# Kernel tuning notes

Hardware: AMD Instinct MI355X
Metric: run time of the kernel (lower is better)

## Reference

```python
import jax, jax.numpy as jnp
import numpy as np

B = 64        # batch
L = 256       # latent_dim
H = 1024      # hidden
D = 1024      # mask dim
BAND = 16     # half-bandwidth of sparsity mask
M = 2 * BAND + 1  # max nnz per row (=33)


def _banded_mask_idx():
    """Build a banded (D,D) 0/1 mask and per-row column indices (D,M), -1 padded."""
    r = np.arange(D)
    mask = (np.abs(r[:, None] - r[None, :]) <= BAND).astype(np.float32)
    idx = np.full((D, M), -1, dtype=np.int32)
    for i in range(D):
        cols = np.nonzero(mask[i])[0]
        idx[i, :len(cols)] = cols
    return mask, idx


def setup_inputs() -> dict:
    key = jax.random.key(0)
    kz, k1, kb1, k2, kb2 = jax.random.split(key, 5)
    mask_np, idx_np = _banded_mask_idx()
    return {
        "z": jax.random.normal(kz, (B, L), dtype=jnp.float32),
        "mask": jnp.asarray(mask_np),
        "W1": jax.random.normal(k1, (L, H), dtype=jnp.float32) * 0.05,
        "b1": jax.random.normal(kb1, (H,), dtype=jnp.float32) * 0.05,
        "W2": jax.random.normal(k2, (H, D * M), dtype=jnp.float32) * 0.02,
        "b2": jax.random.normal(kb2, (D * M,), dtype=jnp.float32) * 0.02,
        "idx": jnp.asarray(idx_np),
    }


def reference(z, mask, W1, b1, W2, b2, idx):
    b = z.shape[0]
    # 2-layer MLP with exact (erf) GELU, as in nn.GELU()
    h = jax.nn.gelu(z @ W1 + b1, approximate=False)
    v = (h @ W2 + b2).reshape(b, D, M)          # (B, D, M)
    # scatter predicted values onto the mask support (unique targets -> add == set)
    valid = idx >= 0                             # (D, M)
    jc = jnp.where(valid, idx, 0)                # clamp -1 padding to col 0
    rows = jnp.broadcast_to(jnp.arange(D)[:, None], (D, M))
    vals = jnp.where(valid, v, jnp.zeros((), v.dtype))
    k = jnp.zeros((b, D, D), dtype=z.dtype).at[:, rows, jc].add(vals)
    # symmetrize, add identity, re-apply mask
    k = 0.5 * (k + jnp.swapaxes(k, -1, -2))
    k = k + jnp.eye(D, dtype=z.dtype)
    return k * mask[None, :, :]
```

## Files before the change

### kernel.cpp

```cpp
#include <hip/hip_runtime.h>
#include <math.h>

#define BATCH 64
#define LDIM  256
#define HDIM  1024
#define DDIM  1024
#define BAND  16
#define MNZ   33
#define NN    (DDIM*MNZ)
#define RTILE 64
#define LSTR  34

typedef float v4f __attribute__((ext_vector_type(4)));

__global__ __launch_bounds__(256) void k1_h(const float* __restrict__ z,
                                            const float* __restrict__ W1,
                                            const float* __restrict__ b1,
                                            float* __restrict__ ht) {
    __shared__ float zs[LDIM];
    const int t = threadIdx.x;
    const int b = blockIdx.y;
    const int j = blockIdx.x * 256 + t;
    zs[t] = z[b * LDIM + t];
    __syncthreads();
    float acc = b1[j];
#pragma unroll 8
    for (int l = 0; l < LDIM; ++l)
        acc = fmaf(zs[l], W1[l * HDIM + j], acc);
    float g = 0.5f * acc * (1.0f + erff(acc * 0.70710678118654752f));
    ht[(size_t)j * BATCH + b] = g;
}

__global__ __launch_bounds__(256) void k2_v(const float* __restrict__ W2,
                                            const float* __restrict__ b2,
                                            const float* __restrict__ ht,
                                            float* __restrict__ vpart,
                                            int kchunk) {
    const int lane = threadIdx.x & 63;
    const int wave = __builtin_amdgcn_readfirstlane((int)(threadIdx.x >> 6));
    const int c0 = blockIdx.x * 256 + lane * 4;
    const int b0 = wave * 16;
    const int ks = blockIdx.y * kchunk;

    v4f acc[16];
#pragma unroll
    for (int j = 0; j < 16; ++j) acc[j] = (v4f){0.f, 0.f, 0.f, 0.f};

    const float* __restrict__ wp = W2 + (size_t)ks * NN + c0;
    const float* __restrict__ hp = ht + (size_t)ks * BATCH + b0;

#pragma unroll 2
    for (int kk = 0; kk < kchunk; ++kk) {
        const v4f w4 = *(const v4f*)(wp + (size_t)kk * NN);
        const float* __restrict__ hh = hp + (size_t)kk * BATCH;
#pragma unroll
        for (int j = 0; j < 16; ++j)
            acc[j] += hh[j] * w4;
    }

    float* __restrict__ vo = vpart + (size_t)blockIdx.y * (BATCH * (size_t)NN)
                             + (size_t)b0 * NN + c0;
    if (blockIdx.y == 0) {
        const v4f bias = *(const v4f*)(b2 + c0);
#pragma unroll
        for (int j = 0; j < 16; ++j)
            *(v4f*)(vo + (size_t)j * NN) = acc[j] + bias;
    } else {
#pragma unroll
        for (int j = 0; j < 16; ++j)
            *(v4f*)(vo + (size_t)j * NN) = acc[j];
    }
}

__global__ __launch_bounds__(256) void k3_out(const float* __restrict__ vpart,
                                              float* __restrict__ out,
                                              int nsplit) {
    const int tid  = threadIdx.x;
    const int tile = blockIdx.x & (DDIM / RTILE - 1);
    const int b    = blockIdx.x / (DDIM / RTILE);
    const int i0 = tile * RTILE;
    const int js = (i0 >= BAND) ? (i0 - BAND) : 0;
    const int je = (i0 + RTILE + BAND <= DDIM) ? (i0 + RTILE + BAND) : DDIM;
    const int nelem = (je - js) * MNZ;

    __shared__ float ls[(RTILE + 2 * BAND) * LSTR];

    const float* __restrict__ vb = vpart + (size_t)b * NN + (size_t)js * MNZ;
    const size_t slice = (size_t)BATCH * NN;
    for (int idx = tid; idx < nelem; idx += 256) {
        const int r = idx / MNZ;
        const int m = idx - r * MNZ;
        float s = vb[idx];
        for (int sl = 1; sl < nsplit; ++sl)
            s += vb[(size_t)sl * slice + idx];
        ls[r * LSTR + m] = s;
    }
    __syncthreads();

    const int j0 = tid * 4;
    for (int r = 0; r < RTILE; ++r) {
        const int i = i0 + r;
        v4f res = (v4f){0.f, 0.f, 0.f, 0.f};
        if (j0 + 3 >= i - BAND && j0 <= i + BAND) {
            const int lo_i = (i > BAND) ? (i - BAND) : 0;
#pragma unroll
            for (int c = 0; c < 4; ++c) {
                const int j = j0 + c;
                const int d = j - i;
                float x = 0.0f;
                if (d >= -BAND && d <= BAND) {
                    const int lo_j = (j > BAND) ? (j - BAND) : 0;
                    x = 0.5f * (ls[(i - js) * LSTR + (j - lo_i)] +
                                ls[(j - js) * LSTR + (i - lo_j)]);
                    if (d == 0) x += 1.0f;
                }
                res[c] = x;
            }
        }
        v4f* dst = ((v4f*)out) + ((size_t)b * DDIM + i) * (DDIM / 4) + tid;
        __builtin_nontemporal_store(res, dst);
    }
}

extern "C" void kernel_launch(void* const* d_in, const int* in_sizes, int n_in,
                              void* d_out, int out_size, void* d_ws, size_t ws_size,
                              hipStream_t stream) {
    const float* z  = (const float*)d_in[0];
    const float* W1 = (const float*)d_in[2];
    const float* b1 = (const float*)d_in[3];
    const float* W2 = (const float*)d_in[4];
    const float* b2 = (const float*)d_in[5];

    float* ht = (float*)d_ws;
    float* vpart = ht + BATCH * HDIM;
    float* out = (float*)d_out;

    const size_t base = (size_t)BATCH * HDIM * sizeof(float);
    const size_t per_slice = (size_t)BATCH * NN * sizeof(float);
    int nsplit = 4;
    while (nsplit > 1 && base + (size_t)nsplit * per_slice > ws_size) nsplit >>= 1;
    const int kchunk = HDIM / nsplit;

    k1_h  <<<dim3(4, 64), 256, 0, stream>>>(z, W1, b1, ht);
    k2_v  <<<dim3(NN / 256, nsplit), 256, 0, stream>>>(W2, b2, ht, vpart, kchunk);
    k3_out<<<dim3(BATCH * (DDIM / RTILE)), 256, 0, stream>>>(vpart, out, nsplit);
}
```

Measured before the change: 476.9 us.

## Stage h chunk in LDS, prefetch W2, and raise split-K to eight

The k2 GEMM now copies its K-chunk of the transposed hidden activations into shared memory and reads it as float4 vectors instead of scalar global loads. It also software-prefetches the next W2 row into a register. The split-K factor is fixed at 8 at compile time, which doubles the grid's y dimension and the number of partial slices the output kernel must sum. The ws_size check that used to pick the split count is gone, so the larger partial buffer may overflow the workspace, and the extra partial traffic may cancel the gains.

```diff
diff --git a/kernel.cpp b/kernel.cpp
--- a/kernel.cpp
+++ b/kernel.cpp
@@ -10,6 +10,8 @@
 #define NN    (DDIM*MNZ)
 #define RTILE 64
 #define LSTR  34
+#define NSPLIT 8
+#define KCHUNK (HDIM / NSPLIT)
 
 typedef float v4f __attribute__((ext_vector_type(4)));
 
@@ -34,28 +36,44 @@
 __global__ __launch_bounds__(256) void k2_v(const float* __restrict__ W2,
                                             const float* __restrict__ b2,
                                             const float* __restrict__ ht,
-                                            float* __restrict__ vpart,
-                                            int kchunk) {
-    const int lane = threadIdx.x & 63;
-    const int wave = __builtin_amdgcn_readfirstlane((int)(threadIdx.x >> 6));
+                                            float* __restrict__ vpart) {
+    __shared__ float lsh[KCHUNK * BATCH];
+    const int tid  = threadIdx.x;
+    const int lane = tid & 63;
+    const int wave = __builtin_amdgcn_readfirstlane(tid >> 6);
     const int c0 = blockIdx.x * 256 + lane * 4;
     const int b0 = wave * 16;
-    const int ks = blockIdx.y * kchunk;
+    const int ks = blockIdx.y * KCHUNK;
+
+    {
+        const v4f* __restrict__ src = (const v4f*)(ht + (size_t)ks * BATCH);
+        v4f* dst = (v4f*)lsh;
+#pragma unroll
+        for (int i = 0; i < (KCHUNK * BATCH) / (4 * 256); ++i)
+            dst[tid + i * 256] = src[tid + i * 256];
+    }
+    __syncthreads();
 
     v4f acc[16];
 #pragma unroll
     for (int j = 0; j < 16; ++j) acc[j] = (v4f){0.f, 0.f, 0.f, 0.f};
 
     const float* __restrict__ wp = W2 + (size_t)ks * NN + c0;
-    const float* __restrict__ hp = ht + (size_t)ks * BATCH + b0;
-
-#pragma unroll 2
-    for (int kk = 0; kk < kchunk; ++kk) {
-        const v4f w4 = *(const v4f*)(wp + (size_t)kk * NN);
-        const float* __restrict__ hh = hp + (size_t)kk * BATCH;
-#pragma unroll
-        for (int j = 0; j < 16; ++j)
-            acc[j] += hh[j] * w4;
+    v4f wnext = *(const v4f*)wp;
+    for (int kk = 0; kk < KCHUNK; ++kk) {
+        const v4f w4 = wnext;
+        const int knext = (kk + 1 < KCHUNK) ? (kk + 1) : (KCHUNK - 1);
+        wnext = *(const v4f*)(wp + (size_t)knext * NN);
+        const v4f* __restrict__ hh = (const v4f*)(lsh + kk * BATCH + b0);
+        const v4f h0 = hh[0], h1 = hh[1], h2 = hh[2], h3 = hh[3];
+        acc[0]  += h0.x * w4;  acc[1]  += h0.y * w4;
+        acc[2]  += h0.z * w4;  acc[3]  += h0.w * w4;
+        acc[4]  += h1.x * w4;  acc[5]  += h1.y * w4;
+        acc[6]  += h1.z * w4;  acc[7]  += h1.w * w4;
+        acc[8]  += h2.x * w4;  acc[9]  += h2.y * w4;
+        acc[10] += h2.z * w4;  acc[11] += h2.w * w4;
+        acc[12] += h3.x * w4;  acc[13] += h3.y * w4;
+        acc[14] += h3.z * w4;  acc[15] += h3.w * w4;
     }
 
     float* __restrict__ vo = vpart + (size_t)blockIdx.y * (BATCH * (size_t)NN)
@@ -73,8 +91,7 @@
 }
 
 __global__ __launch_bounds__(256) void k3_out(const float* __restrict__ vpart,
-                                              float* __restrict__ out,
-                                              int nsplit) {
+                                              float* __restrict__ out) {
     const int tid  = threadIdx.x;
     const int tile = blockIdx.x & (DDIM / RTILE - 1);
     const int b    = blockIdx.x / (DDIM / RTILE);
@@ -90,8 +107,9 @@
     for (int idx = tid; idx < nelem; idx += 256) {
         const int r = idx / MNZ;
         const int m = idx - r * MNZ;
-        float s = vb[idx];
-        for (int sl = 1; sl < nsplit; ++sl)
+        float s = 0.0f;
+#pragma unroll
+        for (int sl = 0; sl < NSPLIT; ++sl)
             s += vb[(size_t)sl * slice + idx];
         ls[r * LSTR + m] = s;
     }
@@ -135,13 +153,7 @@
     float* vpart = ht + BATCH * HDIM;
     float* out = (float*)d_out;
 
-    const size_t base = (size_t)BATCH * HDIM * sizeof(float);
-    const size_t per_slice = (size_t)BATCH * NN * sizeof(float);
-    int nsplit = 4;
-    while (nsplit > 1 && base + (size_t)nsplit * per_slice > ws_size) nsplit >>= 1;
-    const int kchunk = HDIM / nsplit;
-
     k1_h  <<<dim3(4, 64), 256, 0, stream>>>(z, W1, b1, ht);
-    k2_v  <<<dim3(NN / 256, nsplit), 256, 0, stream>>>(W2, b2, ht, vpart, kchunk);
-    k3_out<<<dim3(BATCH * (DDIM / RTILE)), 256, 0, stream>>>(vpart, out, nsplit);
+    k2_v  <<<dim3(NN / 256, NSPLIT), 256, 0, stream>>>(W2, b2, ht, vpart);
+    k3_out<<<dim3(BATCH * (DDIM / RTILE)), 256, 0, stream>>>(vpart, out);
 }
```

After: 535.8 us. +12.3%, slower.
